# Optimization experiments

Hardware: AMD Instinct MI355X
Metric: run time of the kernel (lower is better)

The kernel has to match this reference:

```python
import jax, jax.numpy as jnp
import numpy as np

B = 65536
N = 16            # total agents (1 self + 15 others)
OD = 32           # per_obs_dim
AD = 8            # per_act_dim
H = 128           # num_units_openai
Hh = H // 2       # linear_c0 output
SLOPE = 0.01

def lrelu(x):
    return jax.nn.leaky_relu(x, negative_slope=SLOPE)

def setup_inputs() -> dict:
    key = jax.random.key(0)
    ks = jax.random.split(key, 12)
    def lin(k, fin, fout):
        kw, kb = jax.random.split(k)
        bound = 1.0 / np.sqrt(fin)
        W = jax.random.uniform(kw, (fin, fout), jnp.float32, -bound, bound)
        b = jax.random.uniform(kb, (fout,), jnp.float32, -bound, bound)
        return W, b
    W0, b0 = lin(ks[0], OD + AD, Hh)
    W1, b1 = lin(ks[1], H, 1)
    W2, b2 = lin(ks[2], H, H)
    W3, b3 = lin(ks[3], H, H)
    Wc, bc = lin(ks[4], H, 1)
    obs_input = jax.random.normal(ks[5], (B, N * OD), jnp.float32)
    act_input = jax.random.normal(ks[6], (B, N * AD), jnp.float32)
    return {"obs_input": obs_input, "act_input": act_input,
            "W0": W0, "b0": b0, "W1": W1, "b1": b1,
            "W2": W2, "b2": b2, "W3": W3, "b3": b3,
            "Wc": Wc, "bc": bc}

def reference(obs_input, act_input, W0, b0, W1, b1, W2, b2, W3, b3, Wc, bc):
    obs = obs_input.reshape(B, N, OD)
    act = act_input.reshape(B, N, AD)
    x = jnp.concatenate([obs, act], axis=-1)          # [B, N, OD+AD]
    # shared per-agent transform
    h = jnp.einsum('bnf,fh->bnh', x, W0) + b0         # [B, N, Hh]
    x_self = lrelu(h[:, 0])                           # [B, Hh]
    x_others = jnp.tanh(h[:, 1:])                     # [B, N-1, Hh]
    # attention score: linear_c1 on concat([x_self, x_other]) -> split weight
    a_self = x_self @ W1[:Hh] + b1                    # [B, 1]
    a_oth = jnp.einsum('bnh,ho->bno', x_others, W1[Hh:])  # [B, N-1, 1]
    logits = lrelu(a_self[:, None, :] + a_oth)        # [B, N-1, 1]
    attn = jax.nn.softmax(logits, axis=1)             # softmax over agents
    x_sum = jnp.sum(attn * x_others, axis=1)          # [B, Hh]
    x_cat = jnp.concatenate([x_self, x_sum], axis=1)  # [B, H]
    x1 = lrelu(x_cat @ W2 + b2)
    x2 = lrelu(x1 @ W3 + b3)
    value = x2 @ Wc + bc                              # [B, 1]
    return value
```

## Files before the change

kernel.cpp:

```cpp
#include <hip/hip_runtime.h>
#include <math.h>


#define SLOPE 0.01f
#define LOG2E 1.4426950408889634f

typedef _Float16 f16x8 __attribute__((ext_vector_type(8)));
typedef _Float16 f16x2 __attribute__((ext_vector_type(2)));
typedef __fp16 h16x2 __attribute__((ext_vector_type(2)));
typedef float f32x4 __attribute__((ext_vector_type(4)));

#define MFMA(a, b, c) __builtin_amdgcn_mfma_f32_16x16x32_f16((a), (b), (c), 0, 0, 0)

__device__ __forceinline__ float lrelu(float x) { return fmaxf(x, SLOPE * x); }

__device__ __forceinline__ float fast_tanh(float x) {
    float e = __builtin_amdgcn_exp2f(x * (2.0f * LOG2E));
    float r = __builtin_amdgcn_rcpf(e + 1.0f);
    return fmaf(-2.0f, r, 1.0f);
}

__device__ __forceinline__ f16x8 cvt8(const float f[8]) {
    f16x2 a = __builtin_bit_cast(f16x2, __builtin_amdgcn_cvt_pkrtz(f[0], f[1]));
    f16x2 b = __builtin_bit_cast(f16x2, __builtin_amdgcn_cvt_pkrtz(f[2], f[3]));
    f16x2 c = __builtin_bit_cast(f16x2, __builtin_amdgcn_cvt_pkrtz(f[4], f[5]));
    f16x2 d = __builtin_bit_cast(f16x2, __builtin_amdgcn_cvt_pkrtz(f[6], f[7]));
    f16x8 r;
    r[0] = a[0]; r[1] = a[1]; r[2] = b[0]; r[3] = b[1];
    r[4] = c[0]; r[5] = c[1]; r[6] = d[0]; r[7] = d[1];
    return r;
}

__device__ __forceinline__ float rowsum16(float x) {
    int t;
    t = __builtin_amdgcn_update_dpp(0, __builtin_bit_cast(int, x), 0x121, 0xf, 0xf, true);
    x += __builtin_bit_cast(float, t);
    t = __builtin_amdgcn_update_dpp(0, __builtin_bit_cast(int, x), 0x122, 0xf, 0xf, true);
    x += __builtin_bit_cast(float, t);
    t = __builtin_amdgcn_update_dpp(0, __builtin_bit_cast(int, x), 0x124, 0xf, 0xf, true);
    x += __builtin_bit_cast(float, t);
    t = __builtin_amdgcn_update_dpp(0, __builtin_bit_cast(int, x), 0x128, 0xf, 0xf, true);
    x += __builtin_bit_cast(float, t);
    return x;
}

__global__ __launch_bounds__(256) void pack_weights(
    const float* __restrict__ W0, const float* __restrict__ W2,
    const float* __restrict__ W3, _Float16* __restrict__ ws)
{
    const int g = blockIdx.x * 256 + threadIdx.x;
    if (g >= 4608) return;

    const float* src;
    int ks, ct, lg, lr, ncol, kmax;
    long hoff, loff;
    if (g < 512) {
        ks = g >> 8; ct = (g >> 6) & 3; lg = (g >> 4) & 3; lr = g & 15;
        src = W0; ncol = 64; kmax = 40;
        hoff = (long)g * 8;  loff = hoff + 4096;
    } else if (g < 2560) {
        int gg = g - 512;
        ks = gg >> 9; ct = (gg >> 6) & 7; lg = (gg >> 4) & 3; lr = gg & 15;
        src = W2; ncol = 128; kmax = 128;
        hoff = 8192 + (long)gg * 8; loff = hoff + 16384;
    } else {
        int gg = g - 2560;
        ks = gg >> 9; ct = (gg >> 6) & 7; lg = (gg >> 4) & 3; lr = gg & 15;
        src = W3; ncol = 128; kmax = 128;
        hoff = 40960 + (long)gg * 8; loff = hoff + 16384;
    }

    f16x8 hi, lo;
#pragma unroll
    for (int e = 0; e < 8; ++e) {
        const int k = ks * 32 + lg * 8 + e;
        const float v = (k < kmax) ? src[(long)k * ncol + ct * 16 + lr] : 0.f;
        _Float16 h = (_Float16)v;
        hi[e] = h;
        lo[e] = (_Float16)(v - (float)h);
    }
    *reinterpret_cast<f16x8*>(ws + hoff) = hi;
    *reinterpret_cast<f16x8*>(ws + loff) = lo;
}

__global__ __launch_bounds__(128, 2) void critic_attention_kernel(
    const float* __restrict__ obs, const float* __restrict__ act,
    const float* __restrict__ b0, const float* __restrict__ W1,
    const float* __restrict__ b1v, const float* __restrict__ b2,
    const float* __restrict__ b3, const float* __restrict__ Wc,
    const float* __restrict__ bcv, const _Float16* __restrict__ ws,
    float* __restrict__ out)
{
    __shared__ __align__(16) _Float16 xcat[16 * 136];
    __shared__ float part[16 * 68];
    __shared__ float ps[16];
    __shared__ float vpart[32];

    const int t = threadIdx.x;
    const int lane = t & 63;
    const int w = t >> 6;
    const int lr = lane & 15;
    const int lg = lane >> 4;

    const long ibase = (long)blockIdx.x * 16;

    f16x8 w0h[2][4];
#pragma unroll
    for (int ks = 0; ks < 2; ++ks)
#pragma unroll
        for (int ct = 0; ct < 4; ++ct) {
            const long o = (((long)(ks * 4 + ct) * 4 + lg) * 16 + lr) * 8;
            w0h[ks][ct] = *reinterpret_cast<const f16x8*>(ws + o);
        }

    float b0c[4], W1sc[4], W1oc[4];
#pragma unroll
    for (int ct = 0; ct < 4; ++ct) {
        b0c[ct]  = b0[ct * 16 + lr];
        W1sc[ct] = W1[ct * 16 + lr];
        W1oc[ct] = W1[64 + ct * 16 + lr];
    }
    const float b1s = b1v[0];

    const float* obase = obs + (ibase + lr) * 512 + lg * 8;
    const float* abase = act + (ibase + lr) * 128;

    const int abeg = w ? 8 : 1;
    const int aend = w ? 16 : 8;

    float4 q0 = *reinterpret_cast<const float4*>(obase);
    float4 q1 = *reinterpret_cast<const float4*>(obase + 4);
    float4 c0 = make_float4(0.f, 0.f, 0.f, 0.f), c1 = c0;
    if (lg == 0) {
        c0 = *reinterpret_cast<const float4*>(abase);
        c1 = *reinterpret_cast<const float4*>(abase + 4);
    }

    float a_self[4], s[4], xsum[4][4];
    {
        float f0[8] = {q0.x, q0.y, q0.z, q0.w, q1.x, q1.y, q1.z, q1.w};
        float f1[8] = {c0.x, c0.y, c0.z, c0.w, c1.x, c1.y, c1.z, c1.w};
        f16x8 bi0 = cvt8(f0);
        f16x8 bi1 = cvt8(f1);

        q0 = *reinterpret_cast<const float4*>(obase + abeg * 32);
        q1 = *reinterpret_cast<const float4*>(obase + abeg * 32 + 4);
        if (lg == 0) {
            c0 = *reinterpret_cast<const float4*>(abase + abeg * 8);
            c1 = *reinterpret_cast<const float4*>(abase + abeg * 8 + 4);
        }

        f32x4 acc[4];
#pragma unroll
        for (int ct = 0; ct < 4; ++ct) {
            acc[ct] = (f32x4){b0c[ct], b0c[ct], b0c[ct], b0c[ct]};
            acc[ct] = MFMA(bi0, w0h[0][ct], acc[ct]);
            acc[ct] = MFMA(bi1, w0h[1][ct], acc[ct]);
        }

        float xa[4][4], p[4];
#pragma unroll
        for (int j = 0; j < 4; ++j) {
#pragma unroll
            for (int ct = 0; ct < 4; ++ct)
                xa[ct][j] = lrelu(acc[ct][j]);
            p[j] = xa[0][j] * W1sc[0];
            p[j] = fmaf(xa[1][j], W1sc[1], p[j]);
            p[j] = fmaf(xa[2][j], W1sc[2], p[j]);
            p[j] = fmaf(xa[3][j], W1sc[3], p[j]);
            p[j] = rowsum16(p[j]);
            a_self[j] = b1s + p[j];
            s[j] = 0.f;
#pragma unroll
            for (int ct = 0; ct < 4; ++ct) xsum[ct][j] = 0.f;
        }
        if (w == 0) {
#pragma unroll
            for (int ct = 0; ct < 4; ++ct)
#pragma unroll
                for (int j = 0; j < 4; ++j)
                    xcat[(lg * 4 + j) * 136 + ct * 16 + lr] = (_Float16)xa[ct][j];
        }
    }

    for (int a = abeg; a < aend; ++a) {
        float f0[8] = {q0.x, q0.y, q0.z, q0.w, q1.x, q1.y, q1.z, q1.w};
        float f1[8] = {c0.x, c0.y, c0.z, c0.w, c1.x, c1.y, c1.z, c1.w};
        f16x8 bi0 = cvt8(f0);
        f16x8 bi1 = cvt8(f1);

        if (a + 1 < aend) {
            q0 = *reinterpret_cast<const float4*>(obase + (a + 1) * 32);
            q1 = *reinterpret_cast<const float4*>(obase + (a + 1) * 32 + 4);
            if (lg == 0) {
                c0 = *reinterpret_cast<const float4*>(abase + (a + 1) * 8);
                c1 = *reinterpret_cast<const float4*>(abase + (a + 1) * 8 + 4);
            }
        }

        f32x4 acc[4];
#pragma unroll
        for (int ct = 0; ct < 4; ++ct) {
            acc[ct] = (f32x4){b0c[ct], b0c[ct], b0c[ct], b0c[ct]};
            acc[ct] = MFMA(bi0, w0h[0][ct], acc[ct]);
            acc[ct] = MFMA(bi1, w0h[1][ct], acc[ct]);
        }

        float xa[4][4], p[4];
#pragma unroll
        for (int j = 0; j < 4; ++j) {
#pragma unroll
            for (int ct = 0; ct < 4; ++ct)
                xa[ct][j] = fast_tanh(acc[ct][j]);
            p[j] = xa[0][j] * W1oc[0];
            p[j] = fmaf(xa[1][j], W1oc[1], p[j]);
            p[j] = fmaf(xa[2][j], W1oc[2], p[j]);
            p[j] = fmaf(xa[3][j], W1oc[3], p[j]);
            p[j] = rowsum16(p[j]);
        }
#pragma unroll
        for (int j = 0; j < 4; ++j) {
            const float e = __builtin_amdgcn_exp2f(lrelu(a_self[j] + p[j]) * LOG2E);
            s[j] += e;
#pragma unroll
            for (int ct = 0; ct < 4; ++ct)
                xsum[ct][j] = fmaf(e, xa[ct][j], xsum[ct][j]);
        }
    }

    if (w == 1) {
#pragma unroll
        for (int j = 0; j < 4; ++j) {
#pragma unroll
            for (int ct = 0; ct < 4; ++ct)
                part[(lg * 4 + j) * 68 + ct * 16 + lr] = xsum[ct][j];
            if (lr == 0) ps[lg * 4 + j] = s[j];
        }
    }
    __syncthreads();
    if (w == 0) {
#pragma unroll
        for (int j = 0; j < 4; ++j) {
            const float stot = s[j] + ps[lg * 4 + j];
            const float inv = __builtin_amdgcn_rcpf(stot);
#pragma unroll
            for (int ct = 0; ct < 4; ++ct)
                xcat[(lg * 4 + j) * 136 + 64 + ct * 16 + lr] = (_Float16)(
                    (xsum[ct][j] + part[(lg * 4 + j) * 68 + ct * 16 + lr]) * inv);
        }
    }
    __syncthreads();

    float b2c[4], b3c[4], Wcc[4];
#pragma unroll
    for (int ct = 0; ct < 4; ++ct) {
        const int ctg = w * 4 + ct;
        b2c[ct] = b2[ctg * 16 + lr];
        b3c[ct] = b3[ctg * 16 + lr];
        Wcc[ct] = Wc[ctg * 16 + lr];
    }
    const float bcs = bcv[0];

    f32x4 acc2[4];
#pragma unroll
    for (int ct = 0; ct < 4; ++ct)
        acc2[ct] = (f32x4){b2c[ct], b2c[ct], b2c[ct], b2c[ct]};
#pragma unroll
    for (int ks = 0; ks < 4; ++ks) {
        f16x8 ah = *reinterpret_cast<const f16x8*>(&xcat[lr * 136 + ks * 32 + lg * 8]);
#pragma unroll
        for (int ct = 0; ct < 4; ++ct) {
            const int ctg = w * 4 + ct;
            const long gg = ((long)(ks * 8 + ctg) * 4 + lg) * 16 + lr;
            f16x8 bh = *reinterpret_cast<const f16x8*>(ws + 8192 + gg * 8);
            f16x8 bl = *reinterpret_cast<const f16x8*>(ws + 24576 + gg * 8);
            acc2[ct] = MFMA(ah, bl, acc2[ct]);
            acc2[ct] = MFMA(ah, bh, acc2[ct]);
        }
    }
    __syncthreads();
#pragma unroll
    for (int ct = 0; ct < 4; ++ct)
#pragma unroll
        for (int j = 0; j < 4; ++j)
            xcat[(lg * 4 + j) * 136 + (w * 4 + ct) * 16 + lr] =
                (_Float16)lrelu(acc2[ct][j]);
    __syncthreads();

#pragma unroll
    for (int ct = 0; ct < 4; ++ct)
        acc2[ct] = (f32x4){b3c[ct], b3c[ct], b3c[ct], b3c[ct]};
#pragma unroll
    for (int ks = 0; ks < 4; ++ks) {
        f16x8 ah = *reinterpret_cast<const f16x8*>(&xcat[lr * 136 + ks * 32 + lg * 8]);
#pragma unroll
        for (int ct = 0; ct < 4; ++ct) {
            const int ctg = w * 4 + ct;
            const long gg = ((long)(ks * 8 + ctg) * 4 + lg) * 16 + lr;
            f16x8 bh = *reinterpret_cast<const f16x8*>(ws + 40960 + gg * 8);
            f16x8 bl = *reinterpret_cast<const f16x8*>(ws + 57344 + gg * 8);
            acc2[ct] = MFMA(ah, bl, acc2[ct]);
            acc2[ct] = MFMA(ah, bh, acc2[ct]);
        }
    }

    float v[4];
#pragma unroll
    for (int j = 0; j < 4; ++j) {
        v[j] = lrelu(acc2[0][j]) * Wcc[0];
#pragma unroll
        for (int ct = 1; ct < 4; ++ct)
            v[j] = fmaf(lrelu(acc2[ct][j]), Wcc[ct], v[j]);
        v[j] = rowsum16(v[j]);
    }
    if (lr == 0) {
#pragma unroll
        for (int j = 0; j < 4; ++j)
            vpart[w * 16 + lg * 4 + j] = v[j];
    }
    __syncthreads();
    if (w == 0 && lr == 0) {
#pragma unroll
        for (int j = 0; j < 4; ++j) {
            const int row = lg * 4 + j;
            out[ibase + row] = vpart[row] + vpart[16 + row] + bcs;
        }
    }
}

extern "C" void kernel_launch(void* const* d_in, const int* in_sizes, int n_in,
                              void* d_out, int out_size, void* d_ws, size_t ws_size,
                              hipStream_t stream) {
    (void)in_sizes; (void)n_in; (void)ws_size; (void)out_size;
    const float* obs = (const float*)d_in[0];
    const float* act = (const float*)d_in[1];
    const float* W0  = (const float*)d_in[2];
    const float* b0  = (const float*)d_in[3];
    const float* W1  = (const float*)d_in[4];
    const float* b1  = (const float*)d_in[5];
    const float* W2  = (const float*)d_in[6];
    const float* b2  = (const float*)d_in[7];
    const float* W3  = (const float*)d_in[8];
    const float* b3  = (const float*)d_in[9];
    const float* Wc  = (const float*)d_in[10];
    const float* bc  = (const float*)d_in[11];
    _Float16* ws = (_Float16*)d_ws;

    pack_weights<<<dim3(18), dim3(256), 0, stream>>>(W0, W2, W3, ws);
    critic_attention_kernel<<<dim3(65536 / 16), dim3(128), 0, stream>>>(
        obs, act, b0, W1, b1, b2, b3, Wc, bc, ws, (float*)d_out);
}
```

Baseline: 60.99 us.

## Split each 16-row block across four waves instead of two

Raises the block size from 128 to 256 threads. Agent processing is now spread over four waves (agents 1-4, 5-8, 9-12, 13-15), and the MLP output columns are split so each wave computes 2 column tiles instead of 4. Partial softmax sums and weighted sums from the three extra waves are reduced through enlarged shared buffers. The aim is more parallelism per block and shorter per-wave serial latency. The cost is more shared memory, more cross-wave reduction traffic, and every wave reloading the shared xcat A operands.

```diff
diff --git a/kernel.cpp b/kernel.cpp
--- a/kernel.cpp
+++ b/kernel.cpp
@@ -7,7 +7,6 @@
 
 typedef _Float16 f16x8 __attribute__((ext_vector_type(8)));
 typedef _Float16 f16x2 __attribute__((ext_vector_type(2)));
-typedef __fp16 h16x2 __attribute__((ext_vector_type(2)));
 typedef float f32x4 __attribute__((ext_vector_type(4)));
 
 #define MFMA(a, b, c) __builtin_amdgcn_mfma_f32_16x16x32_f16((a), (b), (c), 0, 0, 0)
@@ -83,7 +82,7 @@
     *reinterpret_cast<f16x8*>(ws + loff) = lo;
 }
 
-__global__ __launch_bounds__(128, 2) void critic_attention_kernel(
+__global__ __launch_bounds__(256, 2) void critic_attention_kernel(
     const float* __restrict__ obs, const float* __restrict__ act,
     const float* __restrict__ b0, const float* __restrict__ W1,
     const float* __restrict__ b1v, const float* __restrict__ b2,
@@ -92,9 +91,9 @@
     float* __restrict__ out)
 {
     __shared__ __align__(16) _Float16 xcat[16 * 136];
-    __shared__ float part[16 * 68];
-    __shared__ float ps[16];
-    __shared__ float vpart[32];
+    __shared__ float part[3][16 * 68];
+    __shared__ float ps[3][16];
+    __shared__ float vpart[4][16];
 
     const int t = threadIdx.x;
     const int lane = t & 63;
@@ -125,8 +124,8 @@
     const float* obase = obs + (ibase + lr) * 512 + lg * 8;
     const float* abase = act + (ibase + lr) * 128;
 
-    const int abeg = w ? 8 : 1;
-    const int aend = w ? 16 : 8;
+    const int abeg = 1 + 4 * w;
+    const int aend = (w == 3) ? 16 : abeg + 4;
 
     float4 q0 = *reinterpret_cast<const float4*>(obase);
     float4 q1 = *reinterpret_cast<const float4*>(obase + 4);
@@ -228,49 +227,52 @@
         }
     }
 
-    if (w == 1) {
-#pragma unroll
-        for (int j = 0; j < 4; ++j) {
-#pragma unroll
-            for (int ct = 0; ct < 4; ++ct)
-                part[(lg * 4 + j) * 68 + ct * 16 + lr] = xsum[ct][j];
-            if (lr == 0) ps[lg * 4 + j] = s[j];
+    if (w >= 1) {
+#pragma unroll
+        for (int j = 0; j < 4; ++j) {
+#pragma unroll
+            for (int ct = 0; ct < 4; ++ct)
+                part[w - 1][(lg * 4 + j) * 68 + ct * 16 + lr] = xsum[ct][j];
+            if (lr == 0) ps[w - 1][lg * 4 + j] = s[j];
         }
     }
     __syncthreads();
     if (w == 0) {
 #pragma unroll
         for (int j = 0; j < 4; ++j) {
-            const float stot = s[j] + ps[lg * 4 + j];
+            const int row = lg * 4 + j;
+            const float stot = s[j] + ps[0][row] + ps[1][row] + ps[2][row];
             const float inv = __builtin_amdgcn_rcpf(stot);
 #pragma unroll
-            for (int ct = 0; ct < 4; ++ct)
-                xcat[(lg * 4 + j) * 136 + 64 + ct * 16 + lr] = (_Float16)(
-                    (xsum[ct][j] + part[(lg * 4 + j) * 68 + ct * 16 + lr]) * inv);
-        }
-    }
-    __syncthreads();
-
-    float b2c[4], b3c[4], Wcc[4];
-#pragma unroll
-    for (int ct = 0; ct < 4; ++ct) {
-        const int ctg = w * 4 + ct;
+            for (int ct = 0; ct < 4; ++ct) {
+                const int o = row * 68 + ct * 16 + lr;
+                const float xs = xsum[ct][j] + part[0][o] + part[1][o] + part[2][o];
+                xcat[row * 136 + 64 + ct * 16 + lr] = (_Float16)(xs * inv);
+            }
+        }
+    }
+    __syncthreads();
+
+    float b2c[2], b3c[2], Wcc[2];
+#pragma unroll
+    for (int ct = 0; ct < 2; ++ct) {
+        const int ctg = w * 2 + ct;
         b2c[ct] = b2[ctg * 16 + lr];
         b3c[ct] = b3[ctg * 16 + lr];
         Wcc[ct] = Wc[ctg * 16 + lr];
     }
     const float bcs = bcv[0];
 
-    f32x4 acc2[4];
-#pragma unroll
-    for (int ct = 0; ct < 4; ++ct)
+    f32x4 acc2[2];
+#pragma unroll
+    for (int ct = 0; ct < 2; ++ct)
         acc2[ct] = (f32x4){b2c[ct], b2c[ct], b2c[ct], b2c[ct]};
 #pragma unroll
     for (int ks = 0; ks < 4; ++ks) {
         f16x8 ah = *reinterpret_cast<const f16x8*>(&xcat[lr * 136 + ks * 32 + lg * 8]);
 #pragma unroll
-        for (int ct = 0; ct < 4; ++ct) {
-            const int ctg = w * 4 + ct;
+        for (int ct = 0; ct < 2; ++ct) {
+            const int ctg = w * 2 + ct;
             const long gg = ((long)(ks * 8 + ctg) * 4 + lg) * 16 + lr;
             f16x8 bh = *reinterpret_cast<const f16x8*>(ws + 8192 + gg * 8);
             f16x8 bl = *reinterpret_cast<const f16x8*>(ws + 24576 + gg * 8);
@@ -280,22 +282,22 @@
     }
     __syncthreads();
 #pragma unroll
-    for (int ct = 0; ct < 4; ++ct)
+    for (int ct = 0; ct < 2; ++ct)
 #pragma unroll
         for (int j = 0; j < 4; ++j)
-            xcat[(lg * 4 + j) * 136 + (w * 4 + ct) * 16 + lr] =
+            xcat[(lg * 4 + j) * 136 + (w * 2 + ct) * 16 + lr] =
                 (_Float16)lrelu(acc2[ct][j]);
     __syncthreads();
 
 #pragma unroll
-    for (int ct = 0; ct < 4; ++ct)
+    for (int ct = 0; ct < 2; ++ct)
         acc2[ct] = (f32x4){b3c[ct], b3c[ct], b3c[ct], b3c[ct]};
 #pragma unroll
     for (int ks = 0; ks < 4; ++ks) {
         f16x8 ah = *reinterpret_cast<const f16x8*>(&xcat[lr * 136 + ks * 32 + lg * 8]);
 #pragma unroll
-        for (int ct = 0; ct < 4; ++ct) {
-            const int ctg = w * 4 + ct;
+        for (int ct = 0; ct < 2; ++ct) {
+            const int ctg = w * 2 + ct;
             const long gg = ((long)(ks * 8 + ctg) * 4 + lg) * 16 + lr;
             f16x8 bh = *reinterpret_cast<const f16x8*>(ws + 40960 + gg * 8);
             f16x8 bl = *reinterpret_cast<const f16x8*>(ws + 57344 + gg * 8);
@@ -308,22 +310,21 @@
 #pragma unroll
     for (int j = 0; j < 4; ++j) {
         v[j] = lrelu(acc2[0][j]) * Wcc[0];
-#pragma unroll
-        for (int ct = 1; ct < 4; ++ct)
-            v[j] = fmaf(lrelu(acc2[ct][j]), Wcc[ct], v[j]);
+        v[j] = fmaf(lrelu(acc2[1][j]), Wcc[1], v[j]);
         v[j] = rowsum16(v[j]);
     }
     if (lr == 0) {
 #pragma unroll
         for (int j = 0; j < 4; ++j)
-            vpart[w * 16 + lg * 4 + j] = v[j];
+            vpart[w][lg * 4 + j] = v[j];
     }
     __syncthreads();
     if (w == 0 && lr == 0) {
 #pragma unroll
         for (int j = 0; j < 4; ++j) {
             const int row = lg * 4 + j;
-            out[ibase + row] = vpart[row] + vpart[16 + row] + bcs;
+            out[ibase + row] = (vpart[0][row] + vpart[1][row]) +
+                               (vpart[2][row] + vpart[3][row]) + bcs;
         }
     }
 }
@@ -347,6 +348,6 @@
     _Float16* ws = (_Float16*)d_ws;
 
     pack_weights<<<dim3(18), dim3(256), 0, stream>>>(W0, W2, W3, ws);
-    critic_attention_kernel<<<dim3(65536 / 16), dim3(128), 0, stream>>>(
+    critic_attention_kernel<<<dim3(65536 / 16), dim3(256), 0, stream>>>(
         obs, act, b0, W1, b1, b2, b3, Wc, bc, ws, (float*)d_out);
 }
```

Measured after the change: 64.63 us. 6.0% more time.

## Process two 16-row tiles per block to reuse weight fragments

Applied to the files above, without the earlier changes.

Each block now handles 32 batch rows as two interleaved 16-row tiles, halving the grid. The W0 fragments in registers and the W2/W3 fragments loaded from global memory are shared across both tiles, and the two independent chains give more instruction-level parallelism to hide load and MFMA latency. The cost is roughly double the accumulator and prefetch registers plus shared memory per block, which may lower occupancy, and half as many blocks to spread across CUs.

```diff
diff --git a/kernel.cpp b/kernel.cpp
--- a/kernel.cpp
+++ b/kernel.cpp
@@ -7,7 +7,6 @@
 
 typedef _Float16 f16x8 __attribute__((ext_vector_type(8)));
 typedef _Float16 f16x2 __attribute__((ext_vector_type(2)));
-typedef __fp16 h16x2 __attribute__((ext_vector_type(2)));
 typedef float f32x4 __attribute__((ext_vector_type(4)));
 
 #define MFMA(a, b, c) __builtin_amdgcn_mfma_f32_16x16x32_f16((a), (b), (c), 0, 0, 0)
@@ -91,10 +90,10 @@
     const float* __restrict__ bcv, const _Float16* __restrict__ ws,
     float* __restrict__ out)
 {
-    __shared__ __align__(16) _Float16 xcat[16 * 136];
-    __shared__ float part[16 * 68];
-    __shared__ float ps[16];
-    __shared__ float vpart[32];
+    __shared__ __align__(16) _Float16 xcat[2][16 * 136];
+    __shared__ float part[2][16 * 68];
+    __shared__ float ps[2][16];
+    __shared__ float vpart[2][2][16];
 
     const int t = threadIdx.x;
     const int lane = t & 63;
@@ -102,7 +101,7 @@
     const int lr = lane & 15;
     const int lg = lane >> 4;
 
-    const long ibase = (long)blockIdx.x * 16;
+    const long ibase = (long)blockIdx.x * 32;
 
     f16x8 w0h[2][4];
 #pragma unroll
@@ -122,32 +121,41 @@
     }
     const float b1s = b1v[0];
 
-    const float* obase = obs + (ibase + lr) * 512 + lg * 8;
-    const float* abase = act + (ibase + lr) * 128;
+    const float* obase[2] = {obs + (ibase + lr) * 512 + lg * 8,
+                             obs + (ibase + 16 + lr) * 512 + lg * 8};
+    const float* abase[2] = {act + (ibase + lr) * 128,
+                             act + (ibase + 16 + lr) * 128};
 
     const int abeg = w ? 8 : 1;
     const int aend = w ? 16 : 8;
 
-    float4 q0 = *reinterpret_cast<const float4*>(obase);
-    float4 q1 = *reinterpret_cast<const float4*>(obase + 4);
-    float4 c0 = make_float4(0.f, 0.f, 0.f, 0.f), c1 = c0;
-    if (lg == 0) {
-        c0 = *reinterpret_cast<const float4*>(abase);
-        c1 = *reinterpret_cast<const float4*>(abase + 4);
-    }
-
-    float a_self[4], s[4], xsum[4][4];
-    {
-        float f0[8] = {q0.x, q0.y, q0.z, q0.w, q1.x, q1.y, q1.z, q1.w};
-        float f1[8] = {c0.x, c0.y, c0.z, c0.w, c1.x, c1.y, c1.z, c1.w};
+    float4 q0[2], q1[2], c0[2], c1[2];
+#pragma unroll
+    for (int tl = 0; tl < 2; ++tl) {
+        q0[tl] = *reinterpret_cast<const float4*>(obase[tl]);
+        q1[tl] = *reinterpret_cast<const float4*>(obase[tl] + 4);
+        c0[tl] = make_float4(0.f, 0.f, 0.f, 0.f); c1[tl] = c0[tl];
+        if (lg == 0) {
+            c0[tl] = *reinterpret_cast<const float4*>(abase[tl]);
+            c1[tl] = *reinterpret_cast<const float4*>(abase[tl] + 4);
+        }
+    }
+
+    float a_self[2][4], s[2][4], xsum[2][4][4];
+#pragma unroll
+    for (int tl = 0; tl < 2; ++tl) {
+        float f0[8] = {q0[tl].x, q0[tl].y, q0[tl].z, q0[tl].w,
+                       q1[tl].x, q1[tl].y, q1[tl].z, q1[tl].w};
+        float f1[8] = {c0[tl].x, c0[tl].y, c0[tl].z, c0[tl].w,
+                       c1[tl].x, c1[tl].y, c1[tl].z, c1[tl].w};
         f16x8 bi0 = cvt8(f0);
         f16x8 bi1 = cvt8(f1);
 
-        q0 = *reinterpret_cast<const float4*>(obase + abeg * 32);
-        q1 = *reinterpret_cast<const float4*>(obase + abeg * 32 + 4);
+        q0[tl] = *reinterpret_cast<const float4*>(obase[tl] + abeg * 32);
+        q1[tl] = *reinterpret_cast<const float4*>(obase[tl] + abeg * 32 + 4);
         if (lg == 0) {
-            c0 = *reinterpret_cast<const float4*>(abase + abeg * 8);
-            c1 = *reinterpret_cast<const float4*>(abase + abeg * 8 + 4);
+            c0[tl] = *reinterpret_cast<const float4*>(abase[tl] + abeg * 8);
+            c1[tl] = *reinterpret_cast<const float4*>(abase[tl] + abeg * 8 + 4);
         }
 
         f32x4 acc[4];
@@ -169,85 +177,96 @@
             p[j] = fmaf(xa[2][j], W1sc[2], p[j]);
             p[j] = fmaf(xa[3][j], W1sc[3], p[j]);
             p[j] = rowsum16(p[j]);
-            a_self[j] = b1s + p[j];
-            s[j] = 0.f;
-#pragma unroll
-            for (int ct = 0; ct < 4; ++ct) xsum[ct][j] = 0.f;
+            a_self[tl][j] = b1s + p[j];
+            s[tl][j] = 0.f;
+#pragma unroll
+            for (int ct = 0; ct < 4; ++ct) xsum[tl][ct][j] = 0.f;
         }
         if (w == 0) {
 #pragma unroll
             for (int ct = 0; ct < 4; ++ct)
 #pragma unroll
                 for (int j = 0; j < 4; ++j)
-                    xcat[(lg * 4 + j) * 136 + ct * 16 + lr] = (_Float16)xa[ct][j];
+                    xcat[tl][(lg * 4 + j) * 136 + ct * 16 + lr] = (_Float16)xa[ct][j];
         }
     }
 
     for (int a = abeg; a < aend; ++a) {
-        float f0[8] = {q0.x, q0.y, q0.z, q0.w, q1.x, q1.y, q1.z, q1.w};
-        float f1[8] = {c0.x, c0.y, c0.z, c0.w, c1.x, c1.y, c1.z, c1.w};
-        f16x8 bi0 = cvt8(f0);
-        f16x8 bi1 = cvt8(f1);
-
-        if (a + 1 < aend) {
-            q0 = *reinterpret_cast<const float4*>(obase + (a + 1) * 32);
-            q1 = *reinterpret_cast<const float4*>(obase + (a + 1) * 32 + 4);
-            if (lg == 0) {
-                c0 = *reinterpret_cast<const float4*>(abase + (a + 1) * 8);
-                c1 = *reinterpret_cast<const float4*>(abase + (a + 1) * 8 + 4);
-            }
-        }
-
-        f32x4 acc[4];
-#pragma unroll
-        for (int ct = 0; ct < 4; ++ct) {
-            acc[ct] = (f32x4){b0c[ct], b0c[ct], b0c[ct], b0c[ct]};
-            acc[ct] = MFMA(bi0, w0h[0][ct], acc[ct]);
-            acc[ct] = MFMA(bi1, w0h[1][ct], acc[ct]);
-        }
-
-        float xa[4][4], p[4];
-#pragma unroll
-        for (int j = 0; j < 4; ++j) {
-#pragma unroll
-            for (int ct = 0; ct < 4; ++ct)
-                xa[ct][j] = fast_tanh(acc[ct][j]);
-            p[j] = xa[0][j] * W1oc[0];
-            p[j] = fmaf(xa[1][j], W1oc[1], p[j]);
-            p[j] = fmaf(xa[2][j], W1oc[2], p[j]);
-            p[j] = fmaf(xa[3][j], W1oc[3], p[j]);
-            p[j] = rowsum16(p[j]);
-        }
-#pragma unroll
-        for (int j = 0; j < 4; ++j) {
-            const float e = __builtin_amdgcn_exp2f(lrelu(a_self[j] + p[j]) * LOG2E);
-            s[j] += e;
-#pragma unroll
-            for (int ct = 0; ct < 4; ++ct)
-                xsum[ct][j] = fmaf(e, xa[ct][j], xsum[ct][j]);
+#pragma unroll
+        for (int tl = 0; tl < 2; ++tl) {
+            float f0[8] = {q0[tl].x, q0[tl].y, q0[tl].z, q0[tl].w,
+                           q1[tl].x, q1[tl].y, q1[tl].z, q1[tl].w};
+            float f1[8] = {c0[tl].x, c0[tl].y, c0[tl].z, c0[tl].w,
+                           c1[tl].x, c1[tl].y, c1[tl].z, c1[tl].w};
+            f16x8 bi0 = cvt8(f0);
+            f16x8 bi1 = cvt8(f1);
+
+            if (a + 1 < aend) {
+                q0[tl] = *reinterpret_cast<const float4*>(obase[tl] + (a + 1) * 32);
+                q1[tl] = *reinterpret_cast<const float4*>(obase[tl] + (a + 1) * 32 + 4);
+                if (lg == 0) {
+                    c0[tl] = *reinterpret_cast<const float4*>(abase[tl] + (a + 1) * 8);
+                    c1[tl] = *reinterpret_cast<const float4*>(abase[tl] + (a + 1) * 8 + 4);
+                }
+            }
+
+            f32x4 acc[4];
+#pragma unroll
+            for (int ct = 0; ct < 4; ++ct) {
+                acc[ct] = (f32x4){b0c[ct], b0c[ct], b0c[ct], b0c[ct]};
+                acc[ct] = MFMA(bi0, w0h[0][ct], acc[ct]);
+                acc[ct] = MFMA(bi1, w0h[1][ct], acc[ct]);
+            }
+
+            float xa[4][4], p[4];
+#pragma unroll
+            for (int j = 0; j < 4; ++j) {
+#pragma unroll
+                for (int ct = 0; ct < 4; ++ct)
+                    xa[ct][j] = fast_tanh(acc[ct][j]);
+                p[j] = xa[0][j] * W1oc[0];
+                p[j] = fmaf(xa[1][j], W1oc[1], p[j]);
+                p[j] = fmaf(xa[2][j], W1oc[2], p[j]);
+                p[j] = fmaf(xa[3][j], W1oc[3], p[j]);
+                p[j] = rowsum16(p[j]);
+            }
+#pragma unroll
+            for (int j = 0; j < 4; ++j) {
+                const float e = __builtin_amdgcn_exp2f(
+                    lrelu(a_self[tl][j] + p[j]) * LOG2E);
+                s[tl][j] += e;
+#pragma unroll
+                for (int ct = 0; ct < 4; ++ct)
+                    xsum[tl][ct][j] = fmaf(e, xa[ct][j], xsum[tl][ct][j]);
+            }
         }
     }
 
     if (w == 1) {
 #pragma unroll
-        for (int j = 0; j < 4; ++j) {
-#pragma unroll
-            for (int ct = 0; ct < 4; ++ct)
-                part[(lg * 4 + j) * 68 + ct * 16 + lr] = xsum[ct][j];
-            if (lr == 0) ps[lg * 4 + j] = s[j];
-        }
+        for (int tl = 0; tl < 2; ++tl)
+#pragma unroll
+            for (int j = 0; j < 4; ++j) {
+#pragma unroll
+                for (int ct = 0; ct < 4; ++ct)
+                    part[tl][(lg * 4 + j) * 68 + ct * 16 + lr] = xsum[tl][ct][j];
+                if (lr == 0) ps[tl][lg * 4 + j] = s[tl][j];
+            }
     }
     __syncthreads();
     if (w == 0) {
 #pragma unroll
-        for (int j = 0; j < 4; ++j) {
-            const float stot = s[j] + ps[lg * 4 + j];
-            const float inv = __builtin_amdgcn_rcpf(stot);
-#pragma unroll
-            for (int ct = 0; ct < 4; ++ct)
-                xcat[(lg * 4 + j) * 136 + 64 + ct * 16 + lr] = (_Float16)(
-                    (xsum[ct][j] + part[(lg * 4 + j) * 68 + ct * 16 + lr]) * inv);
-        }
+        for (int tl = 0; tl < 2; ++tl)
+#pragma unroll
+            for (int j = 0; j < 4; ++j) {
+                const int row = lg * 4 + j;
+                const float stot = s[tl][j] + ps[tl][row];
+                const float inv = __builtin_amdgcn_rcpf(stot);
+#pragma unroll
+                for (int ct = 0; ct < 4; ++ct)
+                    xcat[tl][row * 136 + 64 + ct * 16 + lr] = (_Float16)(
+                        (xsum[tl][ct][j] + part[tl][row * 68 + ct * 16 + lr]) * inv);
+            }
     }
     __syncthreads();
 
@@ -261,70 +280,90 @@
     }
     const float bcs = bcv[0];
 
-    f32x4 acc2[4];
-#pragma unroll
-    for (int ct = 0; ct < 4; ++ct)
-        acc2[ct] = (f32x4){b2c[ct], b2c[ct], b2c[ct], b2c[ct]};
+    f32x4 acc2[2][4];
+#pragma unroll
+    for (int tl = 0; tl < 2; ++tl)
+#pragma unroll
+        for (int ct = 0; ct < 4; ++ct)
+            acc2[tl][ct] = (f32x4){b2c[ct], b2c[ct], b2c[ct], b2c[ct]};
 #pragma unroll
     for (int ks = 0; ks < 4; ++ks) {
-        f16x8 ah = *reinterpret_cast<const f16x8*>(&xcat[lr * 136 + ks * 32 + lg * 8]);
-#pragma unroll
-        for (int ct = 0; ct < 4; ++ct) {
-            const int ctg = w * 4 + ct;
-            const long gg = ((long)(ks * 8 + ctg) * 4 + lg) * 16 + lr;
-            f16x8 bh = *reinterpret_cast<const f16x8*>(ws + 8192 + gg * 8);
-            f16x8 bl = *reinterpret_cast<const f16x8*>(ws + 24576 + gg * 8);
-            acc2[ct] = MFMA(ah, bl, acc2[ct]);
-            acc2[ct] = MFMA(ah, bh, acc2[ct]);
-        }
-    }
-    __syncthreads();
-#pragma unroll
-    for (int ct = 0; ct < 4; ++ct)
-#pragma unroll
-        for (int j = 0; j < 4; ++j)
-            xcat[(lg * 4 + j) * 136 + (w * 4 + ct) * 16 + lr] =
-                (_Float16)lrelu(acc2[ct][j]);
-    __syncthreads();
-
-#pragma unroll
-    for (int ct = 0; ct < 4; ++ct)
-        acc2[ct] = (f32x4){b3c[ct], b3c[ct], b3c[ct], b3c[ct]};
+#pragma unroll
+        for (int tl = 0; tl < 2; ++tl) {
+            f16x8 ah = *reinterpret_cast<const f16x8*>(
+                &xcat[tl][lr * 136 + ks * 32 + lg * 8]);
+#pragma unroll
+            for (int ct = 0; ct < 4; ++ct) {
+                const int ctg = w * 4 + ct;
+                const long gg = ((long)(ks * 8 + ctg) * 4 + lg) * 16 + lr;
+                f16x8 bh = *reinterpret_cast<const f16x8*>(ws + 8192 + gg * 8);
+                f16x8 bl = *reinterpret_cast<const f16x8*>(ws + 24576 + gg * 8);
+                acc2[tl][ct] = MFMA(ah, bl, acc2[tl][ct]);
+                acc2[tl][ct] = MFMA(ah, bh, acc2[tl][ct]);
+            }
+        }
+    }
+    __syncthreads();
+#pragma unroll
+    for (int tl = 0; tl < 2; ++tl)
+#pragma unroll
+        for (int ct = 0; ct < 4; ++ct)
+#pragma unroll
+            for (int j = 0; j < 4; ++j)
+                xcat[tl][(lg * 4 + j) * 136 + (w * 4 + ct) * 16 + lr] =
+                    (_Float16)lrelu(acc2[tl][ct][j]);
+    __syncthreads();
+
+#pragma unroll
+    for (int tl = 0; tl < 2; ++tl)
+#pragma unroll
+        for (int ct = 0; ct < 4; ++ct)
+            acc2[tl][ct] = (f32x4){b3c[ct], b3c[ct], b3c[ct], b3c[ct]};
 #pragma unroll
     for (int ks = 0; ks < 4; ++ks) {
-        f16x8 ah = *reinterpret_cast<const f16x8*>(&xcat[lr * 136 + ks * 32 + lg * 8]);
-#pragma unroll
-        for (int ct = 0; ct < 4; ++ct) {
-            const int ctg = w * 4 + ct;
-            const long gg = ((long)(ks * 8 + ctg) * 4 + lg) * 16 + lr;
-            f16x8 bh = *reinterpret_cast<const f16x8*>(ws + 40960 + gg * 8);
-            f16x8 bl = *reinterpret_cast<const f16x8*>(ws + 57344 + gg * 8);
-            acc2[ct] = MFMA(ah, bl, acc2[ct]);
-            acc2[ct] = MFMA(ah, bh, acc2[ct]);
-        }
-    }
-
-    float v[4];
-#pragma unroll
-    for (int j = 0; j < 4; ++j) {
-        v[j] = lrelu(acc2[0][j]) * Wcc[0];
-#pragma unroll
-        for (int ct = 1; ct < 4; ++ct)
-            v[j] = fmaf(lrelu(acc2[ct][j]), Wcc[ct], v[j]);
-        v[j] = rowsum16(v[j]);
-    }
-    if (lr == 0) {
-#pragma unroll
-        for (int j = 0; j < 4; ++j)
-            vpart[w * 16 + lg * 4 + j] = v[j];
+#pragma unroll
+        for (int tl = 0; tl < 2; ++tl) {
+            f16x8 ah = *reinterpret_cast<const f16x8*>(
+                &xcat[tl][lr * 136 + ks * 32 + lg * 8]);
+#pragma unroll
+            for (int ct = 0; ct < 4; ++ct) {
+                const int ctg = w * 4 + ct;
+                const long gg = ((long)(ks * 8 + ctg) * 4 + lg) * 16 + lr;
+                f16x8 bh = *reinterpret_cast<const f16x8*>(ws + 40960 + gg * 8);
+                f16x8 bl = *reinterpret_cast<const f16x8*>(ws + 57344 + gg * 8);
+                acc2[tl][ct] = MFMA(ah, bl, acc2[tl][ct]);
+                acc2[tl][ct] = MFMA(ah, bh, acc2[tl][ct]);
+            }
+        }
+    }
+
+#pragma unroll
+    for (int tl = 0; tl < 2; ++tl) {
+        float v[4];
+#pragma unroll
+        for (int j = 0; j < 4; ++j) {
+            v[j] = lrelu(acc2[tl][0][j]) * Wcc[0];
+#pragma unroll
+            for (int ct = 1; ct < 4; ++ct)
+                v[j] = fmaf(lrelu(acc2[tl][ct][j]), Wcc[ct], v[j]);
+            v[j] = rowsum16(v[j]);
+        }
+        if (lr == 0) {
+#pragma unroll
+            for (int j = 0; j < 4; ++j)
+                vpart[tl][w][lg * 4 + j] = v[j];
+        }
     }
     __syncthreads();
     if (w == 0 && lr == 0) {
 #pragma unroll
-        for (int j = 0; j < 4; ++j) {
-            const int row = lg * 4 + j;
-            out[ibase + row] = vpart[row] + vpart[16 + row] + bcs;
-        }
+        for (int tl = 0; tl < 2; ++tl)
+#pragma unroll
+            for (int j = 0; j < 4; ++j) {
+                const int row = lg * 4 + j;
+                out[ibase + tl * 16 + row] =
+                    vpart[tl][0][row] + vpart[tl][1][row] + bcs;
+            }
     }
 }
 
@@ -347,6 +386,6 @@
     _Float16* ws = (_Float16*)d_ws;
 
     pack_weights<<<dim3(18), dim3(256), 0, stream>>>(W0, W2, W3, ws);
-    critic_attention_kernel<<<dim3(65536 / 16), dim3(128), 0, stream>>>(
+    critic_attention_kernel<<<dim3(65536 / 32), dim3(128), 0, stream>>>(
         obs, act, b0, W1, b1, b2, b3, Wc, bc, ws, (float*)d_out);
 }
```

New measurement: 57.86 us. 5.1% less time.
